# Kernel tuning notes

Hardware: AMD Instinct MI355X
Metric: run time of the kernel (lower is better)

The kernel has to match this reference:

```python
import jax, jax.numpy as jnp
import numpy as np

N_SRC = 50000
N_DST = 50000
N_EDGES = 800000
D_IN = 128
D_HID = 128
D_OUT = 128


def setup_inputs() -> dict:
    key = jax.random.key(0)
    ks = jax.random.split(key, 8)
    h_src = jax.random.normal(ks[0], (N_SRC, D_IN), dtype=jnp.float32)
    h_dst = jax.random.normal(ks[1], (N_DST, D_IN), dtype=jnp.float32)
    weights = jax.random.uniform(ks[2], (N_EDGES,), dtype=jnp.float32)
    edge_src = jax.random.randint(ks[3], (N_EDGES,), 0, N_SRC, dtype=jnp.int64)
    edge_dst = jax.random.randint(ks[4], (N_EDGES,), 0, N_DST, dtype=jnp.int64)
    # Xavier-uniform-ish init scaled like nn.init.xavier_uniform_(gain=sqrt(2))
    gain = float(np.sqrt(2.0))
    limQ = gain * float(np.sqrt(6.0 / (D_IN + D_HID)))
    limW = gain * float(np.sqrt(6.0 / (D_IN + D_HID + D_OUT)))
    Q_w = jax.random.uniform(ks[5], (D_HID, D_IN), minval=-limQ, maxval=limQ, dtype=jnp.float32)
    Q_b = jnp.zeros((D_HID,), dtype=jnp.float32)
    W_w = jax.random.uniform(ks[6], (D_OUT, D_IN + D_HID), minval=-limW, maxval=limW, dtype=jnp.float32)
    W_b = jnp.zeros((D_OUT,), dtype=jnp.float32)
    return {
        "h_src": h_src, "h_dst": h_dst, "weights": weights,
        "edge_src": edge_src, "edge_dst": edge_dst,
        "Q_w": Q_w, "Q_b": Q_b, "W_w": W_w, "W_b": W_b,
    }


def reference(h_src, h_dst, weights, edge_src, edge_dst, Q_w, Q_b, W_w, W_b):
    # n = relu(Q(h_src))  (dropout is identity in eval mode)
    n_src = jax.nn.relu(h_src @ Q_w.T + Q_b)                    # [N_src, H]
    w = weights.astype(jnp.float32)
    # u_mul_e + sum: weighted message aggregation per destination node
    msgs = n_src[edge_src] * w[:, None]                          # [E, H]
    n = jax.ops.segment_sum(msgs, edge_dst, num_segments=N_DST)  # [N_dst, H]
    # copy_e + sum: per-destination weight sum, clamped at 1
    ws = jax.ops.segment_sum(w, edge_dst, num_segments=N_DST)
    ws = jnp.clip(ws, 1.0, None)[:, None]                        # [N_dst, 1]
    z_in = jnp.concatenate([n / ws, h_dst], axis=1)              # [N_dst, H+D]
    z = jax.nn.relu(z_in @ W_w.T + W_b)                          # [N_dst, O]
    return z
```

## Files before the change

### kernel.cpp

```cpp
#include <hip/hip_runtime.h>
#include <hip/hip_bf16.h>

#define D 128
#define BSHIFT 6
#define BSIZE 64
#define NBUCK 782
#define CAP 1536
#define P1_EPB 4096
#define QPAD 136
#define WPAD 264

typedef __attribute__((ext_vector_type(8))) short bf16x8;
typedef __attribute__((ext_vector_type(4))) float floatx4;

__device__ __forceinline__ unsigned short f2bf(float f) {
    unsigned u = __float_as_uint(f);
    return (unsigned short)((u + 0x7FFFu + ((u >> 16) & 1u)) >> 16);
}
__device__ __forceinline__ float bf2f(unsigned short s) {
    return __uint_as_float(((unsigned)s) << 16);
}

__global__ __launch_bounds__(256)
void fused_g1_p1(const float* __restrict__ h, const float* __restrict__ Qw,
                 const float* __restrict__ Qb, unsigned short* __restrict__ nsrc, int M,
                 const int* __restrict__ esrc, const int* __restrict__ edst,
                 const float* __restrict__ w, int* __restrict__ gcursor,
                 unsigned long long* __restrict__ staging, int E, int G1B) {
    __shared__ unsigned short Bs[128 * QPAD];
    const int tid = threadIdx.x;

    if ((int)blockIdx.x < G1B) {
        const int lane = tid & 63;
        const int wv = tid >> 6;
        const int m0 = (blockIdx.x * 4 + wv) * 16;
        const int rquad = lane >> 4;
        const int rlow = lane & 15;
        const bool active = (m0 < M);

        bf16x8 a[4];
        if (active) {
#pragma unroll
            for (int q = 0; q < 4; ++q) {
                const float* pa = h + (size_t)(m0 + rlow) * D + q * 32 + rquad * 8;
                float4 x = *(const float4*)pa;
                float4 y = *(const float4*)(pa + 4);
                bf16x8 t;
                t[0] = (short)f2bf(x.x); t[1] = (short)f2bf(x.y);
                t[2] = (short)f2bf(x.z); t[3] = (short)f2bf(x.w);
                t[4] = (short)f2bf(y.x); t[5] = (short)f2bf(y.y);
                t[6] = (short)f2bf(y.z); t[7] = (short)f2bf(y.w);
                a[q] = t;
            }
        }

#pragma unroll
        for (int c = tid; c < 4096; c += 256) {
            int row = c >> 5, col4 = (c & 31) * 4;
            float4 x = *(const float4*)(Qw + row * 128 + col4);
            ushort4 t;
            t.x = f2bf(x.x); t.y = f2bf(x.y); t.z = f2bf(x.z); t.w = f2bf(x.w);
            *(ushort4*)&Bs[row * QPAD + col4] = t;
        }
        __syncthreads();
        if (!active) return;

        floatx4 acc[8];
#pragma unroll
        for (int n = 0; n < 8; ++n) acc[n] = (floatx4)0.f;

#pragma unroll
        for (int n = 0; n < 8; ++n) {
#pragma unroll
            for (int q = 0; q < 4; ++q) {
                bf16x8 b = *(const bf16x8*)&Bs[(n * 16 + rlow) * QPAD + q * 32 + rquad * 8];
                acc[n] = __builtin_amdgcn_mfma_f32_16x16x32_bf16(a[q], b, acc[n], 0, 0, 0);
            }
        }

#pragma unroll
        for (int n = 0; n < 8; ++n) {
            int col = n * 16 + rlow;
            float bias = Qb[col];
#pragma unroll
            for (int r = 0; r < 4; ++r) {
                int row = m0 + rquad * 4 + r;
                nsrc[(size_t)row * D + col] = f2bf(fmaxf(acc[n][r] + bias, 0.f));
            }
        }
    } else {
        int* cnt  = (int*)Bs;
        int* base = cnt + NBUCK;
        const int e0 = ((int)blockIdx.x - G1B) * P1_EPB;
        for (int i = tid; i < NBUCK; i += 256) cnt[i] = 0;
        __syncthreads();
#pragma unroll
        for (int i = 0; i < P1_EPB; i += 256) {
            int e = e0 + i + tid;
            if (e < E) atomicAdd(&cnt[edst[e] >> BSHIFT], 1);
        }
        __syncthreads();
        for (int i = tid; i < NBUCK; i += 256) {
            int c = cnt[i];
            base[i] = (c > 0) ? atomicAdd(&gcursor[i], c) : 0;
            cnt[i] = 0;
        }
        __syncthreads();
#pragma unroll
        for (int i = 0; i < P1_EPB; i += 256) {
            int e = e0 + i + tid;
            if (e < E) {
                int d = edst[e];
                int b = d >> BSHIFT;
                int pos = base[b] + atomicAdd(&cnt[b], 1);
                if (pos < CAP) {
                    unsigned long long pk =
                        (unsigned long long)(unsigned)(esrc[e] | ((d & (BSIZE - 1)) << 16)) |
                        ((unsigned long long)__float_as_uint(w[e]) << 32);
                    staging[(size_t)b * CAP + pos] = pk;
                }
            }
        }
    }
}

__global__ __launch_bounds__(256)
void sort_gather(const unsigned long long* __restrict__ staging,
                 const int* __restrict__ gcursor,
                 const unsigned short* __restrict__ nsrc,
                 unsigned short* __restrict__ nout, int N) {
    __shared__ unsigned long long csr[CAP];
    __shared__ int hist[BSIZE], base[BSIZE], cur[BSIZE];
    const int b = blockIdx.x;
    const int tid = threadIdx.x;
    const int cnt = min(gcursor[b], CAP);
    const unsigned long long* st = staging + (size_t)b * CAP;

    if (tid < BSIZE) hist[tid] = 0;
    __syncthreads();
    for (int i = tid; i < cnt; i += 256)
        atomicAdd(&hist[(int)((st[i] >> 16) & (BSIZE - 1))], 1);
    __syncthreads();

    int v = (tid < BSIZE) ? hist[tid] : 0;
    if (tid < BSIZE) base[tid] = v;
    __syncthreads();
#pragma unroll
    for (int off = 1; off < BSIZE; off <<= 1) {
        int t = 0;
        if (tid < BSIZE && tid >= off) t = base[tid - off];
        __syncthreads();
        if (tid < BSIZE) base[tid] += t;
        __syncthreads();
    }
    if (tid < BSIZE) { base[tid] -= v; cur[tid] = 0; }
    __syncthreads();

    for (int i = tid; i < cnt; i += 256) {
        unsigned long long pk = st[i];
        int dl = (int)((pk >> 16) & (BSIZE - 1));
        int slot = base[dl] + atomicAdd(&cur[dl], 1);
        csr[slot] = pk;
    }
    __syncthreads();

    const int wid = tid >> 6, lane = tid & 63;
    const int off2 = lane * 2;
#pragma unroll 1
    for (int k = 0; k < 16; ++k) {
        const int dl = wid * 16 + k;
        const int gnode = b * BSIZE + dl;
        if (gnode >= N) break;
        const int beg = base[dl];
        const int num = hist[dl];

        float a0 = 0.f, a1 = 0.f, a2 = 0.f, a3 = 0.f;
        float ws0 = 0.f, ws1 = 0.f;

        int i = 0;
        for (; i + 8 <= num; i += 8) {
            unsigned long long p[8];
            unsigned vv[8];
            float wt[8];
#pragma unroll
            for (int j = 0; j < 8; ++j) p[j] = csr[beg + i + j];
#pragma unroll
            for (int j = 0; j < 8; ++j) {
                wt[j] = __uint_as_float((unsigned)(p[j] >> 32));
                vv[j] = *(const unsigned*)(nsrc + (size_t)((unsigned)p[j] & 0xFFFFu) * D + off2);
            }
#pragma unroll
            for (int j = 0; j < 8; j += 2) {
                a0 += bf2f((unsigned short)vv[j]) * wt[j];
                a1 += bf2f((unsigned short)(vv[j] >> 16)) * wt[j];
                a2 += bf2f((unsigned short)vv[j + 1]) * wt[j + 1];
                a3 += bf2f((unsigned short)(vv[j + 1] >> 16)) * wt[j + 1];
                ws0 += wt[j]; ws1 += wt[j + 1];
            }
        }
        for (; i + 4 <= num; i += 4) {
            unsigned long long p0 = csr[beg + i + 0], p1 = csr[beg + i + 1];
            unsigned long long p2 = csr[beg + i + 2], p3 = csr[beg + i + 3];
            float w0 = __uint_as_float((unsigned)(p0 >> 32));
            float w1 = __uint_as_float((unsigned)(p1 >> 32));
            float w2 = __uint_as_float((unsigned)(p2 >> 32));
            float w3 = __uint_as_float((unsigned)(p3 >> 32));
            unsigned v0 = *(const unsigned*)(nsrc + (size_t)((unsigned)p0 & 0xFFFFu) * D + off2);
            unsigned v1 = *(const unsigned*)(nsrc + (size_t)((unsigned)p1 & 0xFFFFu) * D + off2);
            unsigned v2 = *(const unsigned*)(nsrc + (size_t)((unsigned)p2 & 0xFFFFu) * D + off2);
            unsigned v3 = *(const unsigned*)(nsrc + (size_t)((unsigned)p3 & 0xFFFFu) * D + off2);
            a0 += bf2f((unsigned short)v0) * w0; a1 += bf2f((unsigned short)(v0 >> 16)) * w0;
            a2 += bf2f((unsigned short)v1) * w1; a3 += bf2f((unsigned short)(v1 >> 16)) * w1;
            a0 += bf2f((unsigned short)v2) * w2; a1 += bf2f((unsigned short)(v2 >> 16)) * w2;
            a2 += bf2f((unsigned short)v3) * w3; a3 += bf2f((unsigned short)(v3 >> 16)) * w3;
            ws0 += w0 + w2; ws1 += w1 + w3;
        }
        for (; i < num; ++i) {
            unsigned long long p = csr[beg + i];
            float wt = __uint_as_float((unsigned)(p >> 32));
            unsigned vv = *(const unsigned*)(nsrc + (size_t)((unsigned)p & 0xFFFFu) * D + off2);
            a0 += bf2f((unsigned short)vv) * wt; a1 += bf2f((unsigned short)(vv >> 16)) * wt;
            ws0 += wt;
        }

        float inv = 1.f / fmaxf(ws0 + ws1, 1.f);
        unsigned outv = (unsigned)f2bf((a0 + a2) * inv) | ((unsigned)f2bf((a1 + a3) * inv) << 16);
        *(unsigned*)(nout + (size_t)gnode * D + off2) = outv;
    }
}

__global__ __launch_bounds__(256)
void gemm2_mfma(const unsigned short* __restrict__ nnorm, const float* __restrict__ hdst,
                const float* __restrict__ Ww, const float* __restrict__ Wb,
                float* __restrict__ out, int M) {
    __shared__ unsigned short Bs[128 * WPAD];
    const int tid = threadIdx.x;
    const int lane = tid & 63;
    const int wv = tid >> 6;
    const int m0 = (blockIdx.x * 4 + wv) * 16;
    const int rquad = lane >> 4;
    const int rlow = lane & 15;
    const bool active = (m0 < M);

    bf16x8 a[8];
    if (active) {
#pragma unroll
        for (int q = 0; q < 4; ++q)
            a[q] = *(const bf16x8*)(nnorm + (size_t)(m0 + rlow) * D + q * 32 + rquad * 8);
#pragma unroll
        for (int q = 4; q < 8; ++q) {
            const float* pa = hdst + (size_t)(m0 + rlow) * D + (q - 4) * 32 + rquad * 8;
            float4 x = *(const float4*)pa;
            float4 y = *(const float4*)(pa + 4);
            bf16x8 t;
            t[0] = (short)f2bf(x.x); t[1] = (short)f2bf(x.y);
            t[2] = (short)f2bf(x.z); t[3] = (short)f2bf(x.w);
            t[4] = (short)f2bf(y.x); t[5] = (short)f2bf(y.y);
            t[6] = (short)f2bf(y.z); t[7] = (short)f2bf(y.w);
            a[q] = t;
        }
    }

#pragma unroll
    for (int c = tid; c < 8192; c += 256) {
        int row = c >> 6, col4 = (c & 63) * 4;
        float4 x = *(const float4*)(Ww + row * 256 + col4);
        ushort4 t;
        t.x = f2bf(x.x); t.y = f2bf(x.y); t.z = f2bf(x.z); t.w = f2bf(x.w);
        *(ushort4*)&Bs[row * WPAD + col4] = t;
    }
    __syncthreads();
    if (!active) return;

    floatx4 acc[8];
#pragma unroll
    for (int n = 0; n < 8; ++n) acc[n] = (floatx4)0.f;

#pragma unroll
    for (int n = 0; n < 8; ++n) {
#pragma unroll
        for (int q = 0; q < 8; ++q) {
            bf16x8 b = *(const bf16x8*)&Bs[(n * 16 + rlow) * WPAD + q * 32 + rquad * 8];
            acc[n] = __builtin_amdgcn_mfma_f32_16x16x32_bf16(a[q], b, acc[n], 0, 0, 0);
        }
    }

#pragma unroll
    for (int n = 0; n < 8; ++n) {
        int col = n * 16 + rlow;
        float bias = Wb[col];
#pragma unroll
        for (int r = 0; r < 4; ++r) {
            int row = m0 + rquad * 4 + r;
            out[(size_t)row * D + col] = fmaxf(acc[n][r] + bias, 0.f);
        }
    }
}

extern "C" void kernel_launch(void* const* d_in, const int* in_sizes, int n_in,
                              void* d_out, int out_size, void* d_ws, size_t ws_size,
                              hipStream_t stream) {
    const float* h_src   = (const float*)d_in[0];
    const float* h_dst   = (const float*)d_in[1];
    const float* weights = (const float*)d_in[2];
    const int*   esrc    = (const int*)d_in[3];
    const int*   edst    = (const int*)d_in[4];
    const float* Q_w     = (const float*)d_in[5];
    const float* Q_b     = (const float*)d_in[6];
    const float* W_w     = (const float*)d_in[7];
    const float* W_b     = (const float*)d_in[8];

    const int N_SRC = in_sizes[0] / D;
    const int N_DST = in_sizes[1] / D;
    const int E     = in_sizes[2];

    char* ws = (char*)d_ws;
    int*  gcursor = (int*)ws;
    unsigned long long* staging = (unsigned long long*)(ws + 4096);
    unsigned short* nsrc16  = (unsigned short*)(ws + 4096 + (size_t)NBUCK * CAP * 8);
    unsigned short* nnorm16 = nsrc16 + (size_t)N_SRC * D;

    float* out = (float*)d_out;

    const int G1B = (N_SRC + 63) / 64;
    const int P1B = (E + P1_EPB - 1) / P1_EPB;

    hipMemsetAsync(gcursor, 0, NBUCK * sizeof(int), stream);

    fused_g1_p1<<<G1B + P1B, 256, 0, stream>>>(h_src, Q_w, Q_b, nsrc16, N_SRC,
                                               esrc, edst, weights, gcursor, staging, E, G1B);

    sort_gather<<<NBUCK, 256, 0, stream>>>(staging, gcursor, nsrc16, nnorm16, N_DST);

    gemm2_mfma<<<(N_DST + 63) / 64, 256, 0, stream>>>(nnorm16, h_dst, W_w, W_b, out, N_DST);
}
```

Measured before the change: 192.8 us.

## Fuse second GEMM into sort-gather kernel and pre-convert W weights to bf16

```diff
diff --git a/kernel.cpp b/kernel.cpp
--- a/kernel.cpp
+++ b/kernel.cpp
@@ -8,7 +8,7 @@
 #define CAP 1536
 #define P1_EPB 4096
 #define QPAD 136
-#define WPAD 264
+#define NNPAD 136
 
 typedef __attribute__((ext_vector_type(8))) short bf16x8;
 typedef __attribute__((ext_vector_type(4))) float floatx4;
@@ -26,7 +26,9 @@
                  const float* __restrict__ Qb, unsigned short* __restrict__ nsrc, int M,
                  const int* __restrict__ esrc, const int* __restrict__ edst,
                  const float* __restrict__ w, int* __restrict__ gcursor,
-                 unsigned long long* __restrict__ staging, int E, int G1B) {
+                 unsigned long long* __restrict__ staging,
+                 const float* __restrict__ Ww, unsigned short* __restrict__ wwbf,
+                 int E, int G1B) {
     __shared__ unsigned short Bs[128 * QPAD];
     const int tid = threadIdx.x;
 
@@ -89,9 +91,16 @@
             }
         }
     } else {
+        const int rb = (int)blockIdx.x - G1B;
+        if (rb < 16) {
+            for (int i = tid; i < 2048; i += 256) {
+                int idx = rb * 2048 + i;
+                wwbf[idx] = f2bf(Ww[idx]);
+            }
+        }
         int* cnt  = (int*)Bs;
         int* base = cnt + NBUCK;
-        const int e0 = ((int)blockIdx.x - G1B) * P1_EPB;
+        const int e0 = rb * P1_EPB;
         for (int i = tid; i < NBUCK; i += 256) cnt[i] = 0;
         __syncthreads();
 #pragma unroll
@@ -125,17 +134,25 @@
 }
 
 __global__ __launch_bounds__(256)
-void sort_gather(const unsigned long long* __restrict__ staging,
-                 const int* __restrict__ gcursor,
-                 const unsigned short* __restrict__ nsrc,
-                 unsigned short* __restrict__ nout, int N) {
+void sg2(const unsigned long long* __restrict__ staging,
+         const int* __restrict__ gcursor,
+         const unsigned short* __restrict__ nsrc,
+         const float* __restrict__ hdst,
+         const unsigned short* __restrict__ wwbf,
+         const float* __restrict__ Wb,
+         float* __restrict__ out, int N) {
     __shared__ unsigned long long csr[CAP];
-    __shared__ int hist[BSIZE], base[BSIZE], cur[BSIZE];
+    __shared__ int hist[BSIZE], base_[BSIZE], cur[BSIZE];
+    __shared__ unsigned short nn[BSIZE][NNPAD];
     const int b = blockIdx.x;
     const int tid = threadIdx.x;
     const int cnt = min(gcursor[b], CAP);
     const unsigned long long* st = staging + (size_t)b * CAP;
 
+    if (b == NBUCK - 1) {
+        unsigned short* f = &nn[0][0];
+        for (int i = tid; i < BSIZE * NNPAD; i += 256) f[i] = 0;
+    }
     if (tid < BSIZE) hist[tid] = 0;
     __syncthreads();
     for (int i = tid; i < cnt; i += 256)
@@ -143,35 +160,36 @@
     __syncthreads();
 
     int v = (tid < BSIZE) ? hist[tid] : 0;
-    if (tid < BSIZE) base[tid] = v;
+    if (tid < BSIZE) base_[tid] = v;
     __syncthreads();
 #pragma unroll
     for (int off = 1; off < BSIZE; off <<= 1) {
         int t = 0;
-        if (tid < BSIZE && tid >= off) t = base[tid - off];
-        __syncthreads();
-        if (tid < BSIZE) base[tid] += t;
-        __syncthreads();
-    }
-    if (tid < BSIZE) { base[tid] -= v; cur[tid] = 0; }
+        if (tid < BSIZE && tid >= off) t = base_[tid - off];
+        __syncthreads();
+        if (tid < BSIZE) base_[tid] += t;
+        __syncthreads();
+    }
+    if (tid < BSIZE) { base_[tid] -= v; cur[tid] = 0; }
     __syncthreads();
 
     for (int i = tid; i < cnt; i += 256) {
         unsigned long long pk = st[i];
         int dl = (int)((pk >> 16) & (BSIZE - 1));
-        int slot = base[dl] + atomicAdd(&cur[dl], 1);
+        int slot = base_[dl] + atomicAdd(&cur[dl], 1);
         csr[slot] = pk;
     }
     __syncthreads();
 
-    const int wid = tid >> 6, lane = tid & 63;
+    const int wv = tid >> 6, lane = tid & 63;
     const int off2 = lane * 2;
+
 #pragma unroll 1
     for (int k = 0; k < 16; ++k) {
-        const int dl = wid * 16 + k;
+        const int dl = wv * 16 + k;
         const int gnode = b * BSIZE + dl;
         if (gnode >= N) break;
-        const int beg = base[dl];
+        const int beg = base_[dl];
         const int num = hist[dl];
 
         float a0 = 0.f, a1 = 0.f, a2 = 0.f, a3 = 0.f;
@@ -225,64 +243,48 @@
 
         float inv = 1.f / fmaxf(ws0 + ws1, 1.f);
         unsigned outv = (unsigned)f2bf((a0 + a2) * inv) | ((unsigned)f2bf((a1 + a3) * inv) << 16);
-        *(unsigned*)(nout + (size_t)gnode * D + off2) = outv;
-    }
-}
-
-__global__ __launch_bounds__(256)
-void gemm2_mfma(const unsigned short* __restrict__ nnorm, const float* __restrict__ hdst,
-                const float* __restrict__ Ww, const float* __restrict__ Wb,
-                float* __restrict__ out, int M) {
-    __shared__ unsigned short Bs[128 * WPAD];
-    const int tid = threadIdx.x;
-    const int lane = tid & 63;
-    const int wv = tid >> 6;
-    const int m0 = (blockIdx.x * 4 + wv) * 16;
-    const int rquad = lane >> 4;
-    const int rlow = lane & 15;
-    const bool active = (m0 < M);
+        *(unsigned*)&nn[dl][off2] = outv;
+    }
+
+    const int rlow = lane & 15, rquad = lane >> 4;
+    const int growA = b * BSIZE + wv * 16 + rlow;
+    const bool validA = (growA < N);
 
     bf16x8 a[8];
-    if (active) {
-#pragma unroll
-        for (int q = 0; q < 4; ++q)
-            a[q] = *(const bf16x8*)(nnorm + (size_t)(m0 + rlow) * D + q * 32 + rquad * 8);
-#pragma unroll
-        for (int q = 4; q < 8; ++q) {
-            const float* pa = hdst + (size_t)(m0 + rlow) * D + (q - 4) * 32 + rquad * 8;
+#pragma unroll
+    for (int q = 0; q < 4; ++q)
+        a[q] = *(const bf16x8*)&nn[wv * 16 + rlow][q * 32 + rquad * 8];
+#pragma unroll
+    for (int q = 4; q < 8; ++q) {
+        bf16x8 t;
+        if (validA) {
+            const float* pa = hdst + (size_t)growA * D + (q - 4) * 32 + rquad * 8;
             float4 x = *(const float4*)pa;
             float4 y = *(const float4*)(pa + 4);
-            bf16x8 t;
             t[0] = (short)f2bf(x.x); t[1] = (short)f2bf(x.y);
             t[2] = (short)f2bf(x.z); t[3] = (short)f2bf(x.w);
             t[4] = (short)f2bf(y.x); t[5] = (short)f2bf(y.y);
             t[6] = (short)f2bf(y.z); t[7] = (short)f2bf(y.w);
-            a[q] = t;
-        }
-    }
-
-#pragma unroll
-    for (int c = tid; c < 8192; c += 256) {
-        int row = c >> 6, col4 = (c & 63) * 4;
-        float4 x = *(const float4*)(Ww + row * 256 + col4);
-        ushort4 t;
-        t.x = f2bf(x.x); t.y = f2bf(x.y); t.z = f2bf(x.z); t.w = f2bf(x.w);
-        *(ushort4*)&Bs[row * WPAD + col4] = t;
-    }
-    __syncthreads();
-    if (!active) return;
+        } else {
+#pragma unroll
+            for (int j = 0; j < 8; ++j) t[j] = 0;
+        }
+        a[q] = t;
+    }
 
     floatx4 acc[8];
 #pragma unroll
     for (int n = 0; n < 8; ++n) acc[n] = (floatx4)0.f;
 
 #pragma unroll
-    for (int n = 0; n < 8; ++n) {
-#pragma unroll
-        for (int q = 0; q < 8; ++q) {
-            bf16x8 b = *(const bf16x8*)&Bs[(n * 16 + rlow) * WPAD + q * 32 + rquad * 8];
-            acc[n] = __builtin_amdgcn_mfma_f32_16x16x32_bf16(a[q], b, acc[n], 0, 0, 0);
-        }
+    for (int q = 0; q < 8; ++q) {
+        bf16x8 bb[8];
+#pragma unroll
+        for (int n = 0; n < 8; ++n)
+            bb[n] = *(const bf16x8*)(wwbf + (size_t)(n * 16 + rlow) * 256 + q * 32 + rquad * 8);
+#pragma unroll
+        for (int n = 0; n < 8; ++n)
+            acc[n] = __builtin_amdgcn_mfma_f32_16x16x32_bf16(a[q], bb[n], acc[n], 0, 0, 0);
     }
 
 #pragma unroll
@@ -291,8 +293,8 @@
         float bias = Wb[col];
 #pragma unroll
         for (int r = 0; r < 4; ++r) {
-            int row = m0 + rquad * 4 + r;
-            out[(size_t)row * D + col] = fmaxf(acc[n][r] + bias, 0.f);
+            int row = b * BSIZE + wv * 16 + rquad * 4 + r;
+            if (row < N) out[(size_t)row * D + col] = fmaxf(acc[n][r] + bias, 0.f);
         }
     }
 }
@@ -317,8 +319,8 @@
     char* ws = (char*)d_ws;
     int*  gcursor = (int*)ws;
     unsigned long long* staging = (unsigned long long*)(ws + 4096);
-    unsigned short* nsrc16  = (unsigned short*)(ws + 4096 + (size_t)NBUCK * CAP * 8);
-    unsigned short* nnorm16 = nsrc16 + (size_t)N_SRC * D;
+    unsigned short* nsrc16 = (unsigned short*)(ws + 4096 + (size_t)NBUCK * CAP * 8);
+    unsigned short* wwbf   = nsrc16 + (size_t)N_SRC * D;
 
     float* out = (float*)d_out;
 
@@ -328,9 +330,8 @@
     hipMemsetAsync(gcursor, 0, NBUCK * sizeof(int), stream);
 
     fused_g1_p1<<<G1B + P1B, 256, 0, stream>>>(h_src, Q_w, Q_b, nsrc16, N_SRC,
-                                               esrc, edst, weights, gcursor, staging, E, G1B);
-
-    sort_gather<<<NBUCK, 256, 0, stream>>>(staging, gcursor, nsrc16, nnorm16, N_DST);
-
-    gemm2_mfma<<<(N_DST + 63) / 64, 256, 0, stream>>>(nnorm16, h_dst, W_w, W_b, out, N_DST);
-}
+                                               esrc, edst, weights, gcursor, staging,
+                                               W_w, wwbf, E, G1B);
+
+    sg2<<<NBUCK, 256, 0, stream>>>(staging, gcursor, nsrc16, h_dst, wwbf, W_b, out, N_DST);
+}
```

Result: slower. 204.2 us (+5.9%).

## Halve dst bucket size and stage W in two halves to shrink LDS

Applied to the files above, without the earlier changes.

```diff
diff --git a/kernel.cpp b/kernel.cpp
--- a/kernel.cpp
+++ b/kernel.cpp
@@ -2,13 +2,13 @@
 #include <hip/hip_bf16.h>
 
 #define D 128
-#define BSHIFT 6
-#define BSIZE 64
-#define NBUCK 782
-#define CAP 1536
+#define BSHIFT 5
+#define BSIZE 32
+#define NBUCK 1563
+#define CAP 768
 #define P1_EPB 4096
 #define QPAD 136
-#define WPAD 264
+#define HPAD 136
 
 typedef __attribute__((ext_vector_type(8))) short bf16x8;
 typedef __attribute__((ext_vector_type(4))) float floatx4;
@@ -130,7 +130,7 @@
                  const unsigned short* __restrict__ nsrc,
                  unsigned short* __restrict__ nout, int N) {
     __shared__ unsigned long long csr[CAP];
-    __shared__ int hist[BSIZE], base[BSIZE], cur[BSIZE];
+    __shared__ int hist[BSIZE], base_[BSIZE], cur[BSIZE];
     const int b = blockIdx.x;
     const int tid = threadIdx.x;
     const int cnt = min(gcursor[b], CAP);
@@ -143,23 +143,23 @@
     __syncthreads();
 
     int v = (tid < BSIZE) ? hist[tid] : 0;
-    if (tid < BSIZE) base[tid] = v;
+    if (tid < BSIZE) base_[tid] = v;
     __syncthreads();
 #pragma unroll
     for (int off = 1; off < BSIZE; off <<= 1) {
         int t = 0;
-        if (tid < BSIZE && tid >= off) t = base[tid - off];
-        __syncthreads();
-        if (tid < BSIZE) base[tid] += t;
-        __syncthreads();
-    }
-    if (tid < BSIZE) { base[tid] -= v; cur[tid] = 0; }
+        if (tid < BSIZE && tid >= off) t = base_[tid - off];
+        __syncthreads();
+        if (tid < BSIZE) base_[tid] += t;
+        __syncthreads();
+    }
+    if (tid < BSIZE) { base_[tid] -= v; cur[tid] = 0; }
     __syncthreads();
 
     for (int i = tid; i < cnt; i += 256) {
         unsigned long long pk = st[i];
         int dl = (int)((pk >> 16) & (BSIZE - 1));
-        int slot = base[dl] + atomicAdd(&cur[dl], 1);
+        int slot = base_[dl] + atomicAdd(&cur[dl], 1);
         csr[slot] = pk;
     }
     __syncthreads();
@@ -167,11 +167,11 @@
     const int wid = tid >> 6, lane = tid & 63;
     const int off2 = lane * 2;
 #pragma unroll 1
-    for (int k = 0; k < 16; ++k) {
-        const int dl = wid * 16 + k;
+    for (int k = 0; k < 8; ++k) {
+        const int dl = wid * 8 + k;
         const int gnode = b * BSIZE + dl;
         if (gnode >= N) break;
-        const int beg = base[dl];
+        const int beg = base_[dl];
         const int num = hist[dl];
 
         float a0 = 0.f, a1 = 0.f, a2 = 0.f, a3 = 0.f;
@@ -233,55 +233,55 @@
 void gemm2_mfma(const unsigned short* __restrict__ nnorm, const float* __restrict__ hdst,
                 const float* __restrict__ Ww, const float* __restrict__ Wb,
                 float* __restrict__ out, int M) {
-    __shared__ unsigned short Bs[128 * WPAD];
+    __shared__ unsigned short Bs[128 * HPAD];
     const int tid = threadIdx.x;
     const int lane = tid & 63;
     const int wv = tid >> 6;
     const int m0 = (blockIdx.x * 4 + wv) * 16;
     const int rquad = lane >> 4;
     const int rlow = lane & 15;
-    const bool active = (m0 < M);
+    const int rr = min(m0 + rlow, M - 1);
 
     bf16x8 a[8];
-    if (active) {
-#pragma unroll
-        for (int q = 0; q < 4; ++q)
-            a[q] = *(const bf16x8*)(nnorm + (size_t)(m0 + rlow) * D + q * 32 + rquad * 8);
-#pragma unroll
-        for (int q = 4; q < 8; ++q) {
-            const float* pa = hdst + (size_t)(m0 + rlow) * D + (q - 4) * 32 + rquad * 8;
-            float4 x = *(const float4*)pa;
-            float4 y = *(const float4*)(pa + 4);
-            bf16x8 t;
-            t[0] = (short)f2bf(x.x); t[1] = (short)f2bf(x.y);
-            t[2] = (short)f2bf(x.z); t[3] = (short)f2bf(x.w);
-            t[4] = (short)f2bf(y.x); t[5] = (short)f2bf(y.y);
-            t[6] = (short)f2bf(y.z); t[7] = (short)f2bf(y.w);
-            a[q] = t;
-        }
-    }
-
-#pragma unroll
-    for (int c = tid; c < 8192; c += 256) {
-        int row = c >> 6, col4 = (c & 63) * 4;
-        float4 x = *(const float4*)(Ww + row * 256 + col4);
-        ushort4 t;
-        t.x = f2bf(x.x); t.y = f2bf(x.y); t.z = f2bf(x.z); t.w = f2bf(x.w);
-        *(ushort4*)&Bs[row * WPAD + col4] = t;
-    }
-    __syncthreads();
-    if (!active) return;
+#pragma unroll
+    for (int q = 0; q < 4; ++q)
+        a[q] = *(const bf16x8*)(nnorm + (size_t)rr * D + q * 32 + rquad * 8);
+#pragma unroll
+    for (int q = 4; q < 8; ++q) {
+        const float* pa = hdst + (size_t)rr * D + (q - 4) * 32 + rquad * 8;
+        float4 x = *(const float4*)pa;
+        float4 y = *(const float4*)(pa + 4);
+        bf16x8 t;
+        t[0] = (short)f2bf(x.x); t[1] = (short)f2bf(x.y);
+        t[2] = (short)f2bf(x.z); t[3] = (short)f2bf(x.w);
+        t[4] = (short)f2bf(y.x); t[5] = (short)f2bf(y.y);
+        t[6] = (short)f2bf(y.z); t[7] = (short)f2bf(y.w);
+        a[q] = t;
+    }
 
     floatx4 acc[8];
 #pragma unroll
     for (int n = 0; n < 8; ++n) acc[n] = (floatx4)0.f;
 
-#pragma unroll
-    for (int n = 0; n < 8; ++n) {
-#pragma unroll
-        for (int q = 0; q < 8; ++q) {
-            bf16x8 b = *(const bf16x8*)&Bs[(n * 16 + rlow) * WPAD + q * 32 + rquad * 8];
-            acc[n] = __builtin_amdgcn_mfma_f32_16x16x32_bf16(a[q], b, acc[n], 0, 0, 0);
+#pragma unroll 1
+    for (int hh = 0; hh < 2; ++hh) {
+        __syncthreads();
+#pragma unroll
+        for (int c = tid; c < 4096; c += 256) {
+            int row = c >> 5, col4 = (c & 31) * 4;
+            float4 x = *(const float4*)(Ww + row * 256 + hh * 128 + col4);
+            ushort4 t;
+            t.x = f2bf(x.x); t.y = f2bf(x.y); t.z = f2bf(x.z); t.w = f2bf(x.w);
+            *(ushort4*)&Bs[row * HPAD + col4] = t;
+        }
+        __syncthreads();
+#pragma unroll
+        for (int n = 0; n < 8; ++n) {
+#pragma unroll
+            for (int q = 0; q < 4; ++q) {
+                bf16x8 b = *(const bf16x8*)&Bs[(n * 16 + rlow) * HPAD + q * 32 + rquad * 8];
+                acc[n] = __builtin_amdgcn_mfma_f32_16x16x32_bf16(a[hh * 4 + q], b, acc[n], 0, 0, 0);
+            }
         }
     }
 
@@ -292,7 +292,7 @@
 #pragma unroll
         for (int r = 0; r < 4; ++r) {
             int row = m0 + rquad * 4 + r;
-            out[(size_t)row * D + col] = fmaxf(acc[n][r] + bias, 0.f);
+            if (row < M) out[(size_t)row * D + col] = fmaxf(acc[n][r] + bias, 0.f);
         }
     }
 }
@@ -316,8 +316,8 @@
 
     char* ws = (char*)d_ws;
     int*  gcursor = (int*)ws;
-    unsigned long long* staging = (unsigned long long*)(ws + 4096);
-    unsigned short* nsrc16  = (unsigned short*)(ws + 4096 + (size_t)NBUCK * CAP * 8);
+    unsigned long long* staging = (unsigned long long*)(ws + 8192);
+    unsigned short* nsrc16  = (unsigned short*)(ws + 8192 + (size_t)NBUCK * CAP * 8);
     unsigned short* nnorm16 = nsrc16 + (size_t)N_SRC * D;
 
     float* out = (float*)d_out;
```

New measurement: 249.2 us. 1.29x slower.
